# Optimization experiments

Hardware: AMD Instinct MI355X
Metric: run time of the kernel (lower is better)

The kernel has to match this reference:

```python
import jax, jax.numpy as jnp
import numpy as np
from jax import lax


def _batch_conv(x, w, b):
    # x: [B, Cin, H, W], w: [B, Cout, Cin, kh, kw], b: [B, Cout]
    # Per-sample conv (the torch code's groups=B grouped-conv trick),
    # expressed as vmap over the batch of an ordinary conv.
    def one(xi, wi):
        return lax.conv_general_dilated(
            xi[None], wi, window_strides=(1, 1), padding='SAME',
            dimension_numbers=('NCHW', 'OIHW', 'NCHW'))[0]
    y = jax.vmap(one)(x, w)                       # [B, Cout, H, W]
    return y + b[:, :, None, None]


def setup_inputs() -> dict:
    key = jax.random.key(0)
    ks = jax.random.split(key, 9)
    B, Cin, H, W = 32, 3, 64, 64
    NC = 10
    s = 0.05
    return {
        'x': jax.random.normal(ks[0], (B, Cin, H, W), jnp.float32),
        'conv1_weight': jax.random.normal(ks[1], (B, 64, Cin, 3, 3), jnp.float32) * s,
        'conv2_weight': jax.random.normal(ks[2], (B, 128, 64, 3, 3), jnp.float32) * s,
        'conv3_weight': jax.random.normal(ks[3], (B, 256, 128, 3, 3), jnp.float32) * s,
        'fc_weight': jax.random.normal(ks[4], (B, 1, NC), jnp.float32) * s,
        'bias1': jax.random.normal(ks[5], (B, 64), jnp.float32) * s,
        'bias2': jax.random.normal(ks[6], (B, 128), jnp.float32) * s,
        'bias3': jax.random.normal(ks[7], (B, 256), jnp.float32) * s,
        'bias4': jax.random.normal(ks[8], (B, NC), jnp.float32) * s,
    }


def reference(x, conv1_weight, conv2_weight, conv3_weight, fc_weight,
              bias1, bias2, bias3, bias4):
    h = jax.nn.relu(_batch_conv(x, conv1_weight, bias1))   # [B, 64, H, W]
    h = jax.nn.relu(_batch_conv(h, conv2_weight, bias2))   # [B, 128, H, W]
    h = jax.nn.relu(_batch_conv(h, conv3_weight, bias3))   # [B, 256, H, W]
    h = jnp.mean(h, axis=(2, 3))                           # AdaptiveAvgPool2d(1) -> [B, 256]
    h = h[:, :, None]                                      # view(B, N, -1) -> [B, 256, 1]
    # BatchLinearLayer: bmm(x, weight) + bias
    out = jnp.einsum('bnd,bdo->bno', h, fc_weight) + bias4[:, None, :]  # [B, 256, 10]
    return out
```

## Files before the change

kernel.cpp:

```cpp
#include <hip/hip_runtime.h>
#include <stdint.h>

typedef __attribute__((ext_vector_type(8))) short short8;
typedef __attribute__((ext_vector_type(16))) float f32x16;

#define NB 32

__device__ __forceinline__ uint16_t f2bf(float f) {
    uint32_t u = __float_as_uint(f);
    u += 0x7fffu + ((u >> 16) & 1u);
    return (uint16_t)(u >> 16);
}

__device__ __forceinline__ void gload16(const void* g, void* l) {
    __builtin_amdgcn_global_load_lds(
        (const __attribute__((address_space(1))) uint32_t*)g,
        (__attribute__((address_space(3))) uint32_t*)l, 16, 0, 0);
}

template<int COUT, int CIN>
__device__ __forceinline__ void prep_w_item(int idx, const float* __restrict__ w,
                                            uint16_t* __restrict__ wp)
{
    const int ci = idx % CIN;
    const int t  = idx / CIN;
    const int oc = t % COUT;
    const int b  = t / COUT;
    const float* s = w + (size_t)idx * 9;
    #pragma unroll
    for (int k = 0; k < 9; k++)
        wp[((size_t)(b * 9 + k) * COUT + oc) * CIN + ci] = f2bf(s[k]);
}

__global__ __launch_bounds__(256) void prep_w3_k(
    const float* __restrict__ w, uint16_t* __restrict__ wp)
{
    const int idx = blockIdx.x * 256 + threadIdx.x;
    if (idx < NB * 256 * 128) prep_w_item<256, 128>(idx, w, wp);
}

template<bool DO_W3>
__global__ __launch_bounds__(256) void prep_all(
    const float* __restrict__ x,  const float* __restrict__ w1,
    const float* __restrict__ w2, const float* __restrict__ w3,
    uint16_t* __restrict__ xp,  uint16_t* __restrict__ wp1,
    uint16_t* __restrict__ wp2, uint16_t* __restrict__ wp3,
    float* __restrict__ zp)
{
    int idx = blockIdx.x * 256 + threadIdx.x;
    if (idx < 4096) {
        ((float4*)zp)[idx] = make_float4(0.f, 0.f, 0.f, 0.f);
        return;
    }
    idx -= 4096;
    if (idx < 131072) {
        const int xc = idx & 63, y = (idx >> 6) & 63, b = idx >> 12;
        const float* s = x + (size_t)b * 3 * 4096 + y * 64 + xc;
        const uint16_t v0 = f2bf(s[0]), v1 = f2bf(s[4096]), v2 = f2bf(s[8192]);
        short8 lo = {(short)v0, (short)v1, (short)v2, 0, 0, 0, 0, 0};
        short8 hi = {0, 0, 0, 0, 0, 0, 0, 0};
        uint16_t* d = xp + (size_t)idx * 16;
        *(short8*)d = lo;
        *(short8*)(d + 8) = hi;
        return;
    }
    idx -= 131072;
    if (idx < 18432) {
        const int oc = idx & 63, k = (idx >> 6) % 9, b = idx / 576;
        const uint16_t v0 = f2bf(w1[((size_t)(b * 64 + oc) * 3 + 0) * 9 + k]);
        const uint16_t v1 = f2bf(w1[((size_t)(b * 64 + oc) * 3 + 1) * 9 + k]);
        const uint16_t v2 = f2bf(w1[((size_t)(b * 64 + oc) * 3 + 2) * 9 + k]);
        short8 lo = {(short)v0, (short)v1, (short)v2, 0, 0, 0, 0, 0};
        short8 hi = {0, 0, 0, 0, 0, 0, 0, 0};
        uint16_t* d = wp1 + ((size_t)(b * 9 + k) * 64 + oc) * 16;
        *(short8*)d = lo;
        *(short8*)(d + 8) = hi;
        return;
    }
    idx -= 18432;
    if (idx < 262144) {
        prep_w_item<128, 64>(idx, w2, wp2);
        return;
    }
    if (!DO_W3) return;
    idx -= 262144;
    if (idx < 1048576) prep_w_item<256, 128>(idx, w3, wp3);
}

template<int CIN, int COUT, int OCBLKS, bool POOL>
__global__ __launch_bounds__(256, 2) void conv_mfma(
    const uint16_t* __restrict__ in, const uint16_t* __restrict__ wp,
    const float* __restrict__ bias, uint16_t* __restrict__ out,
    float* __restrict__ partial, const float* __restrict__ zp)
{
    constexpr int IN_GA = 1344;
    constexpr int W_G   = 1152;
    constexpr int IN_B  = IN_GA * 16;
    constexpr int BUF_B = IN_B + W_G * 16;
    constexpr int P     = OCBLKS * 8;
    extern __shared__ __align__(16) char sm[];

    const int L   = blockIdx.x;
    const int xcd = L & 7;
    const int jj  = L >> 3;
    const int b   = (jj / P) * 8 + xcd;
    const int inner = jj % P;
    const int ocbase = (inner >> 3) * 64;
    const int stripe = inner & 7;
    const int y0 = stripe * 8;

    const int tid = threadIdx.x;
    const int wv = tid >> 6, l = tid & 63, q = l >> 5, ln = l & 31;
    const int NK = CIN / 16;

    const uint16_t* src_in[6];
    #pragma unroll
    for (int i = 0; i < 6; i++) {
        const int gp = i * 256 + tid;
        const int rq = gp / 66, px = gp - rq * 66;
        const int row = rq >> 1, qq = rq & 1;
        const int gy = y0 - 1 + row, gx = px - 1;
        const bool valid = (rq < 20) && ((unsigned)gy < 64u) && ((unsigned)gx < 64u);
        src_in[i] = valid ? in + ((size_t)((b * 64 + gy) * 64 + gx) * CIN + qq * 8)
                          : (const uint16_t*)zp;
    }
    const uint16_t* src_w[5];
    #pragma unroll
    for (int i = 0; i < 5; i++) {
        const int gp = i * 256 + tid;
        const int kq = gp >> 6, oc = gp & 63;
        const int kk = kq >> 1, qq = kq & 1;
        src_w[i] = wp + ((size_t)(b * 9 + kk) * COUT + ocbase + oc) * CIN + qq * 8;
    }

    int aoff[4][2];
    #pragma unroll
    for (int t = 0; t < 4; t++)
        #pragma unroll
        for (int h = 0; h < 2; h++)
            aoff[t][h] = ((((wv * 2 + t) * 2 + q) * 66) + h * 32 + ln) * 16;
    const int qoff = q * 1024 + ln * 16;

    f32x16 aA0, aA1, aB0, aB1, aC0, aC1, aD0, aD1;
    {
        const float bv0 = bias[b * COUT + ocbase + ln];
        const float bv1 = bias[b * COUT + ocbase + 32 + ln];
        #pragma unroll
        for (int r = 0; r < 16; r++) {
            aA0[r] = bv0; aB0[r] = bv0; aC0[r] = bv0; aD0[r] = bv0;
            aA1[r] = bv1; aB1[r] = bv1; aC1[r] = bv1; aD1[r] = bv1;
        }
    }

    auto stage = [&](char* base, int k) {
        const int koff = k * 16;
        #pragma unroll
        for (int i = 0; i < 6; i++) {
            const int g0 = i * 256 + wv * 64;
            if (g0 < IN_GA) gload16(src_in[i] + koff, base + g0 * 16);
        }
        #pragma unroll
        for (int i = 0; i < 5; i++) {
            const int g0 = i * 256 + wv * 64;
            if (g0 < W_G) gload16(src_w[i] + koff, base + IN_B + g0 * 16);
        }
    };

    stage(sm, 0);
    asm volatile("s_waitcnt vmcnt(0)" ::: "memory");
    __syncthreads();

    for (int k = 0; k < NK; k++) {
        const char* cb = sm + (k & 1) * BUF_B;
        if (k + 1 < NK) stage(sm + ((k + 1) & 1) * BUF_B, k + 1);
        __builtin_amdgcn_s_setprio(1);
        #pragma unroll
        for (int ky = 0; ky < 3; ky++)
            #pragma unroll
            for (int kx = 0; kx < 3; kx++) {
                const int kk = ky * 3 + kx;
                short8 fA = *(const short8*)(cb + aoff[ky][0] + kx * 16);
                short8 fB = *(const short8*)(cb + aoff[ky][1] + kx * 16);
                short8 fC = *(const short8*)(cb + aoff[ky + 1][0] + kx * 16);
                short8 fD = *(const short8*)(cb + aoff[ky + 1][1] + kx * 16);
                const char* bw = cb + IN_B + kk * 2048 + qoff;
                short8 b0 = *(const short8*)(bw);
                short8 b1 = *(const short8*)(bw + 512);
                aA0 = __builtin_amdgcn_mfma_f32_32x32x16_bf16(fA, b0, aA0, 0, 0, 0);
                aB0 = __builtin_amdgcn_mfma_f32_32x32x16_bf16(fB, b0, aB0, 0, 0, 0);
                aC0 = __builtin_amdgcn_mfma_f32_32x32x16_bf16(fC, b0, aC0, 0, 0, 0);
                aD0 = __builtin_amdgcn_mfma_f32_32x32x16_bf16(fD, b0, aD0, 0, 0, 0);
                aA1 = __builtin_amdgcn_mfma_f32_32x32x16_bf16(fA, b1, aA1, 0, 0, 0);
                aB1 = __builtin_amdgcn_mfma_f32_32x32x16_bf16(fB, b1, aB1, 0, 0, 0);
                aC1 = __builtin_amdgcn_mfma_f32_32x32x16_bf16(fC, b1, aC1, 0, 0, 0);
                aD1 = __builtin_amdgcn_mfma_f32_32x32x16_bf16(fD, b1, aD1, 0, 0, 0);
            }
        __builtin_amdgcn_s_setprio(0);
        asm volatile("s_waitcnt vmcnt(0)" ::: "memory");
        __syncthreads();
    }

    if (!POOL) {
        #pragma unroll
        for (int r = 0; r < 16; r++) {
            const int pxr = (r & 3) + 8 * (r >> 2) + 4 * q;
            const int y0w = y0 + wv * 2;
            uint16_t* dA = out + (size_t)((b * 64 + y0w) * 64 + pxr) * COUT + ocbase;
            uint16_t* dB = out + (size_t)((b * 64 + y0w) * 64 + 32 + pxr) * COUT + ocbase;
            uint16_t* dC = out + (size_t)((b * 64 + y0w + 1) * 64 + pxr) * COUT + ocbase;
            uint16_t* dD = out + (size_t)((b * 64 + y0w + 1) * 64 + 32 + pxr) * COUT + ocbase;
            dA[ln]      = f2bf(fmaxf(aA0[r], 0.f));
            dA[32 + ln] = f2bf(fmaxf(aA1[r], 0.f));
            dB[ln]      = f2bf(fmaxf(aB0[r], 0.f));
            dB[32 + ln] = f2bf(fmaxf(aB1[r], 0.f));
            dC[ln]      = f2bf(fmaxf(aC0[r], 0.f));
            dC[32 + ln] = f2bf(fmaxf(aC1[r], 0.f));
            dD[ln]      = f2bf(fmaxf(aD0[r], 0.f));
            dD[32 + ln] = f2bf(fmaxf(aD1[r], 0.f));
        }
    } else {
        float* red = (float*)(sm + 2 * BUF_B);
        float s0 = 0.f, s1 = 0.f;
        #pragma unroll
        for (int r = 0; r < 16; r++) {
            s0 += fmaxf(aA0[r], 0.f) + fmaxf(aB0[r], 0.f)
                + fmaxf(aC0[r], 0.f) + fmaxf(aD0[r], 0.f);
            s1 += fmaxf(aA1[r], 0.f) + fmaxf(aB1[r], 0.f)
                + fmaxf(aC1[r], 0.f) + fmaxf(aD1[r], 0.f);
        }
        s0 += __shfl_xor(s0, 32);
        s1 += __shfl_xor(s1, 32);
        if (q == 0) {
            red[wv * 64 + ln] = s0;
            red[wv * 64 + 32 + ln] = s1;
        }
        __syncthreads();
        if (tid < 64) {
            float t = red[tid] + red[64 + tid] + red[128 + tid] + red[192 + tid];
            partial[(size_t)(b * 256 + ocbase + tid) * 8 + stripe] = t;
        }
    }
}

__global__ void fc_k(const float* __restrict__ partial,
                     const float* __restrict__ fcw,
                     const float* __restrict__ b4, float* __restrict__ out)
{
    const int b = blockIdx.x, c = threadIdx.x;
    const float* p = partial + (size_t)(b * 256 + c) * 8;
    float s = 0.f;
    #pragma unroll
    for (int i = 0; i < 8; i++) s += p[i];
    const float pooled = s * (1.f / 4096.f);
    #pragma unroll
    for (int o = 0; o < 10; o++)
        out[(b * 256 + c) * 10 + o] = fmaf(pooled, fcw[b * 10 + o], b4[b * 10 + o]);
}

extern "C" void kernel_launch(void* const* d_in, const int* in_sizes, int n_in,
                              void* d_out, int out_size, void* d_ws, size_t ws_size,
                              hipStream_t stream)
{
    const float* x   = (const float*)d_in[0];
    const float* w1  = (const float*)d_in[1];
    const float* w2  = (const float*)d_in[2];
    const float* w3  = (const float*)d_in[3];
    const float* fcw = (const float*)d_in[4];
    const float* b1  = (const float*)d_in[5];
    const float* b2  = (const float*)d_in[6];
    const float* b3  = (const float*)d_in[7];
    const float* b4  = (const float*)d_in[8];
    char* ws = (char*)d_ws;
    uint16_t* xp  = (uint16_t*)(ws);
    uint16_t* wp1 = (uint16_t*)(ws + 4194304);
    uint16_t* h2  = (uint16_t*)(ws);
    uint16_t* h1  = (uint16_t*)(ws + 33554432);
    uint16_t* wp2 = (uint16_t*)(ws + 50331648);
    const bool big_ws = ws_size >= 74186752u;
    uint16_t* wp3     = (uint16_t*)(ws + (big_ws ? 55050240u : 33554432u));
    float*    partial = (float*)   (ws + (big_ws ? 73924608u : 52428800u));
    float*    zp      = (float*)d_out;

    constexpr int DYN_LDS = 2 * 39936 + 1024;
    static bool attr_done = false;
    if (!attr_done) {
        hipFuncSetAttribute((const void*)&conv_mfma<16, 64, 1, false>,
                            hipFuncAttributeMaxDynamicSharedMemorySize, DYN_LDS);
        hipFuncSetAttribute((const void*)&conv_mfma<64, 128, 2, false>,
                            hipFuncAttributeMaxDynamicSharedMemorySize, DYN_LDS);
        hipFuncSetAttribute((const void*)&conv_mfma<128, 256, 4, true>,
                            hipFuncAttributeMaxDynamicSharedMemorySize, DYN_LDS);
        attr_done = true;
    }

    if (big_ws) {
        prep_all<true><<<5720, 256, 0, stream>>>(x, w1, w2, w3, xp, wp1, wp2, wp3, zp);
    } else {
        prep_all<false><<<1624, 256, 0, stream>>>(x, w1, w2, w3, xp, wp1, wp2, wp3, zp);
    }
    conv_mfma<16, 64, 1, false><<<NB * 8, 256, DYN_LDS, stream>>>(xp, wp1, b1, h1, nullptr, zp);
    conv_mfma<64, 128, 2, false><<<NB * 16, 256, DYN_LDS, stream>>>(h1, wp2, b2, h2, nullptr, zp);
    if (!big_ws)
        prep_w3_k<<<4096, 256, 0, stream>>>(w3, wp3);
    conv_mfma<128, 256, 4, true><<<NB * 32, 256, DYN_LDS, stream>>>(h2, wp3, b3, nullptr, partial, zp);
    fc_k<<<NB, 256, 0, stream>>>(partial, fcw, b4, (float*)d_out);
}
```

Measured before the change: 129.0 us.

## Restructure conv K-loop into per-row phases with batched LDS reads and barriers

```diff
diff --git a/kernel.cpp b/kernel.cpp
--- a/kernel.cpp
+++ b/kernel.cpp
@@ -172,32 +172,45 @@
 
     for (int k = 0; k < NK; k++) {
         const char* cb = sm + (k & 1) * BUF_B;
-        if (k + 1 < NK) stage(sm + ((k + 1) & 1) * BUF_B, k + 1);
-        __builtin_amdgcn_s_setprio(1);
-        #pragma unroll
-        for (int ky = 0; ky < 3; ky++)
+        #pragma unroll
+        for (int ph = 0; ph < 3; ph++) {
+            short8 fA[2][2][3];
+            short8 fB[2][3];
+            #pragma unroll
+            for (int dr = 0; dr < 2; dr++)
+                #pragma unroll
+                for (int h = 0; h < 2; h++)
+                    #pragma unroll
+                    for (int kx = 0; kx < 3; kx++)
+                        fA[dr][h][kx] = *(const short8*)(cb + aoff[ph + dr][h] + kx * 16);
             #pragma unroll
             for (int kx = 0; kx < 3; kx++) {
-                const int kk = ky * 3 + kx;
-                short8 fA = *(const short8*)(cb + aoff[ky][0] + kx * 16);
-                short8 fB = *(const short8*)(cb + aoff[ky][1] + kx * 16);
-                short8 fC = *(const short8*)(cb + aoff[ky + 1][0] + kx * 16);
-                short8 fD = *(const short8*)(cb + aoff[ky + 1][1] + kx * 16);
-                const char* bw = cb + IN_B + kk * 2048 + qoff;
-                short8 b0 = *(const short8*)(bw);
-                short8 b1 = *(const short8*)(bw + 512);
-                aA0 = __builtin_amdgcn_mfma_f32_32x32x16_bf16(fA, b0, aA0, 0, 0, 0);
-                aB0 = __builtin_amdgcn_mfma_f32_32x32x16_bf16(fB, b0, aB0, 0, 0, 0);
-                aC0 = __builtin_amdgcn_mfma_f32_32x32x16_bf16(fC, b0, aC0, 0, 0, 0);
-                aD0 = __builtin_amdgcn_mfma_f32_32x32x16_bf16(fD, b0, aD0, 0, 0, 0);
-                aA1 = __builtin_amdgcn_mfma_f32_32x32x16_bf16(fA, b1, aA1, 0, 0, 0);
-                aB1 = __builtin_amdgcn_mfma_f32_32x32x16_bf16(fB, b1, aB1, 0, 0, 0);
-                aC1 = __builtin_amdgcn_mfma_f32_32x32x16_bf16(fC, b1, aC1, 0, 0, 0);
-                aD1 = __builtin_amdgcn_mfma_f32_32x32x16_bf16(fD, b1, aD1, 0, 0, 0);
+                const char* bw = cb + IN_B + (ph * 3 + kx) * 2048 + qoff;
+                fB[0][kx] = *(const short8*)(bw);
+                fB[1][kx] = *(const short8*)(bw + 512);
             }
-        __builtin_amdgcn_s_setprio(0);
-        asm volatile("s_waitcnt vmcnt(0)" ::: "memory");
-        __syncthreads();
+            if (ph == 0 && k + 1 < NK)
+                stage(sm + ((k + 1) & 1) * BUF_B, k + 1);
+            __builtin_amdgcn_s_barrier();
+            asm volatile("s_waitcnt lgkmcnt(0)" ::: "memory");
+            __builtin_amdgcn_sched_barrier(0);
+            __builtin_amdgcn_s_setprio(1);
+            #pragma unroll
+            for (int kx = 0; kx < 3; kx++) {
+                aA0 = __builtin_amdgcn_mfma_f32_32x32x16_bf16(fA[0][0][kx], fB[0][kx], aA0, 0, 0, 0);
+                aB0 = __builtin_amdgcn_mfma_f32_32x32x16_bf16(fA[0][1][kx], fB[0][kx], aB0, 0, 0, 0);
+                aC0 = __builtin_amdgcn_mfma_f32_32x32x16_bf16(fA[1][0][kx], fB[0][kx], aC0, 0, 0, 0);
+                aD0 = __builtin_amdgcn_mfma_f32_32x32x16_bf16(fA[1][1][kx], fB[0][kx], aD0, 0, 0, 0);
+                aA1 = __builtin_amdgcn_mfma_f32_32x32x16_bf16(fA[0][0][kx], fB[1][kx], aA1, 0, 0, 0);
+                aB1 = __builtin_amdgcn_mfma_f32_32x32x16_bf16(fA[0][1][kx], fB[1][kx], aB1, 0, 0, 0);
+                aC1 = __builtin_amdgcn_mfma_f32_32x32x16_bf16(fA[1][0][kx], fB[1][kx], aC1, 0, 0, 0);
+                aD1 = __builtin_amdgcn_mfma_f32_32x32x16_bf16(fA[1][1][kx], fB[1][kx], aD1, 0, 0, 0);
+            }
+            __builtin_amdgcn_s_setprio(0);
+            if (ph == 2)
+                asm volatile("s_waitcnt vmcnt(0)" ::: "memory");
+            __builtin_amdgcn_s_barrier();
+        }
     }
 
     if (!POOL) {
```

After: 128.6 us. Within noise of the previous version (-0.3%).
